# Kernel tuning notes

Measured on AMD Instinct MI355X. Metric: run time of the kernel, lower is better.

## Reference

```python
import jax, jax.numpy as jnp
import numpy as np


def setup_inputs() -> dict:
    key = jax.random.key(0)
    k1, k2 = jax.random.split(key)
    B, N, S, C = 8, 65536, 4, 8
    psi = jax.random.normal(k1, (B, N, S), dtype=jnp.float32)
    # nn.Parameter(torch.randn(d_coord, d_spinor, d_spinor) / sqrt(d_spinor))
    gamma = jax.random.normal(k2, (C, S, S), dtype=jnp.float32) / jnp.sqrt(jnp.float32(S))
    return {"psi": psi, "gamma": gamma}


def reference(psi, gamma):
    # G[mu,nu] = gamma[mu] @ gamma[nu]  -> [C, C, S, S]
    G = jnp.einsum('mij,njk->mnik', gamma, gamma)
    Gt = jnp.swapaxes(G, 0, 1)                 # G[nu,mu]
    A = 0.5 * (G - Gt)                         # 0.5 * commutator  (K1 generator)
    Ssym = 0.5 * (G + Gt)                      # 0.5 * anticommutator (K2 generator)

    # K0: sigma = psi_bar psi (psi_bar == psi here)
    K0 = jnp.einsum('bni,bni->bn', psi, psi)   # [B, N]

    # Precompute small outer product per token, then contract once per output.
    outer = jnp.einsum('bni,bnj->bnij', psi, psi)   # [B, N, S, S] (small S=4)
    K1 = jnp.einsum('bnij,mnuv->bnmn'.replace('nu', 'x'), outer, A) if False else \
         jnp.einsum('bnij,cdij->bncd', outer, A)    # [B, N, C, C] antisymmetric
    K2 = jnp.einsum('bnij,cdij->bncd', outer, Ssym) # [B, N, C, C] symmetric
    return (K0, K1, K2)
```

## Files before the change

### kernel.cpp

```cpp
#include <hip/hip_runtime.h>


#define TPB 256
#define TOK 64
#define STRIDE 68

typedef float f32x4 __attribute__((ext_vector_type(4)));

__device__ __forceinline__ float dot4(float4 a, float4 b) {
    return a.x * b.x + a.y * b.y + a.z * b.z + a.w * b.w;
}

__global__ __launch_bounds__(TPB) void spinor_bilinears_v4(
    const float* __restrict__ psi,
    const float* __restrict__ gamma,
    float* __restrict__ out,
    long long n_tokens) {
    __shared__ float ldsT[TOK * STRIDE];

    const int tid = threadIdx.x;
    const int wave = tid >> 6;
    const int lane = tid & 63;

    if (wave < 2) {
        const long long t = (long long)blockIdx.x * TOK + lane;
        const float4 p = ((const float4*)psi)[t];
        if (wave == 0) {
            __builtin_nontemporal_store(dot4(p, p), &out[t]);
        }
        const float4* g4 = (const float4*)gamma;

        float4 v[8];
#pragma unroll
        for (int d = 0; d < 8; ++d) {
            const float4 g0 = g4[d * 4 + 0];
            const float4 g1 = g4[d * 4 + 1];
            const float4 g2 = g4[d * 4 + 2];
            const float4 g3 = g4[d * 4 + 3];
            float4 vd;
            vd.x = dot4(g0, p);
            vd.y = dot4(g1, p);
            vd.z = dot4(g2, p);
            vd.w = dot4(g3, p);
            v[d] = vd;
        }

        float* trow = &ldsT[lane * STRIDE];
#pragma unroll
        for (int i = 0; i < 4; ++i) {
            const int c = wave * 4 + i;
            const float4 g0 = g4[c * 4 + 0];
            const float4 g1 = g4[c * 4 + 1];
            const float4 g2 = g4[c * 4 + 2];
            const float4 g3 = g4[c * 4 + 3];
            float4 u;
            u.x = p.x * g0.x + p.y * g1.x + p.z * g2.x + p.w * g3.x;
            u.y = p.x * g0.y + p.y * g1.y + p.z * g2.y + p.w * g3.y;
            u.z = p.x * g0.z + p.y * g1.z + p.z * g2.z + p.w * g3.z;
            u.w = p.x * g0.w + p.y * g1.w + p.z * g2.w + p.w * g3.w;
            f32x4 q0, q1;
            q0[0] = dot4(u, v[0]); q0[1] = dot4(u, v[1]);
            q0[2] = dot4(u, v[2]); q0[3] = dot4(u, v[3]);
            q1[0] = dot4(u, v[4]); q1[1] = dot4(u, v[5]);
            q1[2] = dot4(u, v[6]); q1[3] = dot4(u, v[7]);
            *(f32x4*)(trow + c * 8 + 0) = q0;
            *(f32x4*)(trow + c * 8 + 4) = q1;
        }
    }

    __syncthreads();

    const long long blk = (long long)blockIdx.x * (TOK * 16);
    f32x4* K1v = (f32x4*)(out + n_tokens) + blk;
    f32x4* K2v = (f32x4*)(out + n_tokens + n_tokens * 64) + blk;

#pragma unroll
    for (int it = 0; it < 4; ++it) {
        const int item = it * TPB + tid;
        const int tl = item >> 4;
        const int cd0 = (item & 15) * 4;
        const int c = cd0 >> 3;
        const int d0 = cd0 & 7;
        const float* trow = &ldsT[tl * STRIDE];

        const f32x4 tcd = *(const f32x4*)(trow + cd0);
        const float td0 = trow[(d0 + 0) * 8 + c];
        const float td1 = trow[(d0 + 1) * 8 + c];
        const float td2 = trow[(d0 + 2) * 8 + c];
        const float td3 = trow[(d0 + 3) * 8 + c];

        f32x4 o1, o2;
        o1[0] = 0.5f * (tcd[0] - td0);  o2[0] = 0.5f * (tcd[0] + td0);
        o1[1] = 0.5f * (tcd[1] - td1);  o2[1] = 0.5f * (tcd[1] + td1);
        o1[2] = 0.5f * (tcd[2] - td2);  o2[2] = 0.5f * (tcd[2] + td2);
        o1[3] = 0.5f * (tcd[3] - td3);  o2[3] = 0.5f * (tcd[3] + td3);

        __builtin_nontemporal_store(o1, &K1v[item]);
        __builtin_nontemporal_store(o2, &K2v[item]);
    }
}

extern "C" void kernel_launch(void* const* d_in, const int* in_sizes, int n_in,
                              void* d_out, int out_size, void* d_ws, size_t ws_size,
                              hipStream_t stream) {
    const float* psi = (const float*)d_in[0];
    const float* gamma = (const float*)d_in[1];
    float* out = (float*)d_out;

    const long long n_tokens = (long long)in_sizes[0] / 4;
    const int blocks = (int)(n_tokens / TOK);

    spinor_bilinears_v4<<<blocks, TPB, 0, stream>>>(psi, gamma, out, n_tokens);
}
```

Before: 272.2 us.

## Convert to persistent grid-stride kernel with prefetched psi loads

The kernel now launches a fixed grid of 2048 blocks, and each block loops over token chunks grid-stride instead of handling one chunk per block. The next chunk's psi is loaded into registers right after the first barrier, so that load overlaps the transpose and store phase. This removes per-block launch and setup overhead for the 8192 chunks. In exchange it adds a second barrier per iteration, and a fixed grid may reduce the number of stores in flight.

```diff
diff --git a/kernel.cpp b/kernel.cpp
--- a/kernel.cpp
+++ b/kernel.cpp
@@ -4,6 +4,7 @@
 #define TPB 256
 #define TOK 64
 #define STRIDE 68
+#define GRID 2048
 
 typedef float f32x4 __attribute__((ext_vector_type(4)));
 
@@ -11,7 +12,7 @@
     return a.x * b.x + a.y * b.y + a.z * b.z + a.w * b.w;
 }
 
-__global__ __launch_bounds__(TPB) void spinor_bilinears_v4(
+__global__ __launch_bounds__(TPB) void spinor_bilinears_v5(
     const float* __restrict__ psi,
     const float* __restrict__ gamma,
     float* __restrict__ out,
@@ -21,82 +22,92 @@
     const int tid = threadIdx.x;
     const int wave = tid >> 6;
     const int lane = tid & 63;
+    const long long nchunks = n_tokens / TOK;
 
+    const float4* __restrict__ psi4 = (const float4*)psi;
+    const float4* __restrict__ g4 = (const float4*)gamma;
+    f32x4* K1 = (f32x4*)(out + n_tokens);
+    f32x4* K2 = (f32x4*)(out + n_tokens + n_tokens * 64);
+
+    float4 p = make_float4(0.f, 0.f, 0.f, 0.f);
     if (wave < 2) {
-        const long long t = (long long)blockIdx.x * TOK + lane;
-        const float4 p = ((const float4*)psi)[t];
-        if (wave == 0) {
-            __builtin_nontemporal_store(dot4(p, p), &out[t]);
+        p = psi4[(long long)blockIdx.x * TOK + lane];
+    }
+
+    for (long long chunk = blockIdx.x; chunk < nchunks; chunk += GRID) {
+        if (wave < 2) {
+            const long long t = chunk * TOK + lane;
+            if (wave == 0) {
+                __builtin_nontemporal_store(dot4(p, p), &out[t]);
+            }
+            float4 v[8];
+#pragma unroll
+            for (int d = 0; d < 8; ++d) {
+                const float4 g0 = g4[d * 4 + 0];
+                const float4 g1 = g4[d * 4 + 1];
+                const float4 g2 = g4[d * 4 + 2];
+                const float4 g3 = g4[d * 4 + 3];
+                float4 vd;
+                vd.x = dot4(g0, p);
+                vd.y = dot4(g1, p);
+                vd.z = dot4(g2, p);
+                vd.w = dot4(g3, p);
+                v[d] = vd;
+            }
+            float* trow = &ldsT[lane * STRIDE];
+#pragma unroll
+            for (int i = 0; i < 4; ++i) {
+                const int c = wave * 4 + i;
+                const float4 g0 = g4[c * 4 + 0];
+                const float4 g1 = g4[c * 4 + 1];
+                const float4 g2 = g4[c * 4 + 2];
+                const float4 g3 = g4[c * 4 + 3];
+                float4 u;
+                u.x = p.x * g0.x + p.y * g1.x + p.z * g2.x + p.w * g3.x;
+                u.y = p.x * g0.y + p.y * g1.y + p.z * g2.y + p.w * g3.y;
+                u.z = p.x * g0.z + p.y * g1.z + p.z * g2.z + p.w * g3.z;
+                u.w = p.x * g0.w + p.y * g1.w + p.z * g2.w + p.w * g3.w;
+                f32x4 q0, q1;
+                q0[0] = dot4(u, v[0]); q0[1] = dot4(u, v[1]);
+                q0[2] = dot4(u, v[2]); q0[3] = dot4(u, v[3]);
+                q1[0] = dot4(u, v[4]); q1[1] = dot4(u, v[5]);
+                q1[2] = dot4(u, v[6]); q1[3] = dot4(u, v[7]);
+                *(f32x4*)(trow + c * 8 + 0) = q0;
+                *(f32x4*)(trow + c * 8 + 4) = q1;
+            }
         }
-        const float4* g4 = (const float4*)gamma;
+        __syncthreads();
 
-        float4 v[8];
-#pragma unroll
-        for (int d = 0; d < 8; ++d) {
-            const float4 g0 = g4[d * 4 + 0];
-            const float4 g1 = g4[d * 4 + 1];
-            const float4 g2 = g4[d * 4 + 2];
-            const float4 g3 = g4[d * 4 + 3];
-            float4 vd;
-            vd.x = dot4(g0, p);
-            vd.y = dot4(g1, p);
-            vd.z = dot4(g2, p);
-            vd.w = dot4(g3, p);
-            v[d] = vd;
+        if (wave < 2 && chunk + GRID < nchunks) {
+            p = psi4[(chunk + GRID) * TOK + lane];
         }
 
-        float* trow = &ldsT[lane * STRIDE];
+        const long long blkq = chunk * (TOK * 16);
 #pragma unroll
-        for (int i = 0; i < 4; ++i) {
-            const int c = wave * 4 + i;
-            const float4 g0 = g4[c * 4 + 0];
-            const float4 g1 = g4[c * 4 + 1];
-            const float4 g2 = g4[c * 4 + 2];
-            const float4 g3 = g4[c * 4 + 3];
-            float4 u;
-            u.x = p.x * g0.x + p.y * g1.x + p.z * g2.x + p.w * g3.x;
-            u.y = p.x * g0.y + p.y * g1.y + p.z * g2.y + p.w * g3.y;
-            u.z = p.x * g0.z + p.y * g1.z + p.z * g2.z + p.w * g3.z;
-            u.w = p.x * g0.w + p.y * g1.w + p.z * g2.w + p.w * g3.w;
-            f32x4 q0, q1;
-            q0[0] = dot4(u, v[0]); q0[1] = dot4(u, v[1]);
-            q0[2] = dot4(u, v[2]); q0[3] = dot4(u, v[3]);
-            q1[0] = dot4(u, v[4]); q1[1] = dot4(u, v[5]);
-            q1[2] = dot4(u, v[6]); q1[3] = dot4(u, v[7]);
-            *(f32x4*)(trow + c * 8 + 0) = q0;
-            *(f32x4*)(trow + c * 8 + 4) = q1;
+        for (int it = 0; it < 4; ++it) {
+            const int item = it * TPB + tid;
+            const int tl = item >> 4;
+            const int cd0 = (item & 15) * 4;
+            const int cc = cd0 >> 3;
+            const int d0 = cd0 & 7;
+            const float* trow = &ldsT[tl * STRIDE];
+
+            const f32x4 tcd = *(const f32x4*)(trow + cd0);
+            const float td0 = trow[(d0 + 0) * 8 + cc];
+            const float td1 = trow[(d0 + 1) * 8 + cc];
+            const float td2 = trow[(d0 + 2) * 8 + cc];
+            const float td3 = trow[(d0 + 3) * 8 + cc];
+
+            f32x4 o1, o2;
+            o1[0] = 0.5f * (tcd[0] - td0);  o2[0] = 0.5f * (tcd[0] + td0);
+            o1[1] = 0.5f * (tcd[1] - td1);  o2[1] = 0.5f * (tcd[1] + td1);
+            o1[2] = 0.5f * (tcd[2] - td2);  o2[2] = 0.5f * (tcd[2] + td2);
+            o1[3] = 0.5f * (tcd[3] - td3);  o2[3] = 0.5f * (tcd[3] + td3);
+
+            __builtin_nontemporal_store(o1, &K1[blkq + item]);
+            __builtin_nontemporal_store(o2, &K2[blkq + item]);
         }
-    }
-
-    __syncthreads();
-
-    const long long blk = (long long)blockIdx.x * (TOK * 16);
-    f32x4* K1v = (f32x4*)(out + n_tokens) + blk;
-    f32x4* K2v = (f32x4*)(out + n_tokens + n_tokens * 64) + blk;
-
-#pragma unroll
-    for (int it = 0; it < 4; ++it) {
-        const int item = it * TPB + tid;
-        const int tl = item >> 4;
-        const int cd0 = (item & 15) * 4;
-        const int c = cd0 >> 3;
-        const int d0 = cd0 & 7;
-        const float* trow = &ldsT[tl * STRIDE];
-
-        const f32x4 tcd = *(const f32x4*)(trow + cd0);
-        const float td0 = trow[(d0 + 0) * 8 + c];
-        const float td1 = trow[(d0 + 1) * 8 + c];
-        const float td2 = trow[(d0 + 2) * 8 + c];
-        const float td3 = trow[(d0 + 3) * 8 + c];
-
-        f32x4 o1, o2;
-        o1[0] = 0.5f * (tcd[0] - td0);  o2[0] = 0.5f * (tcd[0] + td0);
-        o1[1] = 0.5f * (tcd[1] - td1);  o2[1] = 0.5f * (tcd[1] + td1);
-        o1[2] = 0.5f * (tcd[2] - td2);  o2[2] = 0.5f * (tcd[2] + td2);
-        o1[3] = 0.5f * (tcd[3] - td3);  o2[3] = 0.5f * (tcd[3] + td3);
-
-        __builtin_nontemporal_store(o1, &K1v[item]);
-        __builtin_nontemporal_store(o2, &K2v[item]);
+        __syncthreads();
     }
 }
 
@@ -108,7 +119,6 @@
     float* out = (float*)d_out;
 
     const long long n_tokens = (long long)in_sizes[0] / 4;
-    const int blocks = (int)(n_tokens / TOK);
 
-    spinor_bilinears_v4<<<blocks, TPB, 0, stream>>>(psi, gamma, out, n_tokens);
+    spinor_bilinears_v5<<<GRID, TPB, 0, stream>>>(psi, gamma, out, n_tokens);
 }
```

Measured after the change: 276.0 us. About the same (+1.4%).
